# Performance work log

Hardware: AMD Instinct MI355X
Metric: run time of the kernel (lower is better)

## Reference

```python
import jax, jax.numpy as jnp
import numpy as np
import math

DIM = 512
HEADS = 8
DH = DIM // HEADS
B, C, H, W = 2, 512, 48, 48


def setup_inputs() -> dict:
    key = jax.random.key(0)
    k1, k2, k3, k4 = jax.random.split(key, 4)
    x = jax.random.normal(k1, (B, C, H, W), dtype=jnp.float32)
    # torch Linear weights: [out_features, in_features]
    w_qkv = jax.random.normal(k2, (3 * DIM, DIM), dtype=jnp.float32) * (DIM ** -0.5)
    w_out = jax.random.normal(k3, (DIM, DIM), dtype=jnp.float32) * (DIM ** -0.5)
    b_out = jax.random.normal(k4, (DIM,), dtype=jnp.float32) * 0.01
    wavelength = jnp.asarray(0.1, dtype=jnp.float32)
    return {"x": x, "w_qkv": w_qkv, "w_out": w_out, "b_out": b_out, "wavelength": wavelength}


def reference(x, w_qkv, w_out, b_out, wavelength):
    b, c, h, w = x.shape
    n = h * w
    scale = DH ** -0.5

    x_flat = x.reshape(b, c, n).transpose(0, 2, 1)  # [B, N, C]
    qkv = jnp.einsum('bnc,dc->bnd', x_flat, w_qkv)   # [B, N, 3*DIM]
    q, k, v = jnp.split(qkv, 3, axis=-1)

    def to_heads(t):
        return t.reshape(b, n, HEADS, DH).transpose(0, 2, 1, 3)  # [B, h, N, dh]

    q, k, v = to_heads(q), to_heads(k), to_heads(v)

    dots = jnp.einsum('bhid,bhjd->bhij', q, k) * scale  # [B, h, N, N]

    # Fresnel interference bias over spatial positions
    yy, xx = jnp.meshgrid(jnp.arange(h), jnp.arange(w), indexing='ij')
    positions = jnp.stack([yy, xx], axis=-1).astype(jnp.float32).reshape(-1, 2)  # [N, 2]
    pos_diff = positions[None, :, :] - positions[:, None, :]  # [N, N, 2]
    distances = jnp.sqrt(jnp.sum(pos_diff ** 2, axis=-1) + 1e-8)  # [N, N]
    phase = 2.0 * math.pi * distances / (jnp.abs(wavelength) * h + 1e-6)
    interference = jnp.cos(phase)

    dots = dots + interference[None, None, :, :] * 0.1
    attn = jax.nn.softmax(dots, axis=-1)
    out = jnp.einsum('bhij,bhjd->bhid', attn, v)  # [B, h, N, dh]
    out = out.transpose(0, 2, 1, 3).reshape(b, n, HEADS * DH)  # [B, N, DIM]
    out = jnp.einsum('bnd,od->bno', out, w_out) + b_out
    return out.transpose(0, 2, 1).reshape(b, c, h, w)
```

## Files before the change

### kernel.cpp

```cpp
#include <hip/hip_runtime.h>
#include <math.h>

#define BB 2
#define CC 512
#define NN 2304
#define NH 8
#define DD 512
#define D3 1536
#define WIDTH 48
#define C1 0.18033688f

#define KSPLIT 2
#define KTILES 18
#define NTBL 213

typedef _Float16 h8 __attribute__((ext_vector_type(8)));
typedef _Float16 h4 __attribute__((ext_vector_type(4)));
typedef _Float16 h2 __attribute__((ext_vector_type(2)));
typedef float f4 __attribute__((ext_vector_type(4)));

__device__ __forceinline__ void gload16(const void* g, void* s) {
  __builtin_amdgcn_global_load_lds(
      (const __attribute__((address_space(1))) unsigned int*)g,
      (__attribute__((address_space(3))) unsigned int*)s, 16, 0, 0);
}

__global__ __launch_bounds__(256) void prep_k(
    const float* __restrict__ x, const float* __restrict__ wq,
    const float* __restrict__ wo, const float* __restrict__ wavp,
    _Float16* __restrict__ xt, _Float16* __restrict__ wqh,
    _Float16* __restrict__ woh, _Float16* __restrict__ btf)
{
  __shared__ float Ls[32][33];
  const int t = threadIdx.x;
  const int e = blockIdx.x;

  if (e < 2304) {
    const int n0 = (e % 72) * 32;
    const int c0 = ((e / 72) % 16) * 32;
    const int b  = e / 1152;
#pragma unroll
    for (int p = 0; p < 4; ++p) {
      const int cl = (t >> 5) + p * 8, nl = t & 31;
      Ls[cl][nl] = x[((size_t)b * CC + c0 + cl) * NN + n0 + nl];
    }
    __syncthreads();
#pragma unroll
    for (int p = 0; p < 2; ++p) {
      const int nl = (t >> 4) + p * 16, cl = (t & 15) * 2;
      h2 v = {(_Float16)Ls[cl][nl], (_Float16)Ls[cl + 1][nl]};
      *(h2*)(xt + ((size_t)b * NN + n0 + nl) * CC + c0 + cl) = v;
    }
  } else if (e < 3328) {
    const int idx = (e - 2304) * 256 + t;
    const int NQ = (D3 * CC) / 4;
    if (idx < NQ) {
      float4 v = *(const float4*)(wq + (size_t)idx * 4);
      h4 o = {(_Float16)v.x, (_Float16)v.y, (_Float16)v.z, (_Float16)v.w};
      *(h4*)(wqh + (size_t)idx * 4) = o;
    } else {
      const int j = idx - NQ;
      float4 v = *(const float4*)(wo + (size_t)j * 4);
      h4 o = {(_Float16)v.x, (_Float16)v.y, (_Float16)v.z, (_Float16)v.w};
      *(h4*)(woh + (size_t)j * 4) = o;
    }
  } else {
    const int tbl = (e - 3328) * 2 + (t >> 7);
    if (tbl < NTBL) {
      const int tid = t & 127;
      const int dD = tbl / 3, qm = tbl % 3;
      const int qt0 = qm + 36;
      const int kt0 = qt0 - (dD - 35);
      const int w = tid >> 6, quad = (tid >> 4) & 3, l15 = tid & 15;
      const float pc = 6.283185307179586f / (fabsf(wavp[0]) * (float)WIDTH + 1e-6f);
      _Float16* o = btf + ((size_t)tbl * 128 + tid) * 32;
#pragma unroll
      for (int g = 0; g < 4; ++g) {
        h8 v;
#pragma unroll
        for (int el = 0; el < 8; ++el) {
          const int j = g * 8 + el;
          const int nt = j >> 4, mt = (j >> 2) & 3, r = j & 3;
          const int q = qt0 * 64 + w * 32 + nt * 16 + l15;
          const int k = kt0 * 64 + mt * 16 + quad * 4 + r;
          const float dy = (float)(q / WIDTH) - (float)(k / WIDTH);
          const float dx = (float)(q % WIDTH) - (float)(k % WIDTH);
          const float dist = sqrtf(dy * dy + dx * dx + 1e-8f);
          v[el] = (_Float16)(0.1f * __cosf(dist * pc) * 1.44269504f);
        }
        *(h8*)(o + g * 8) = v;
      }
    }
  }
}

__global__ __launch_bounds__(256) void qkv_gemm_k(
    const _Float16* __restrict__ xt, const _Float16* __restrict__ wqh,
    _Float16* __restrict__ qb, _Float16* __restrict__ kb,
    _Float16* __restrict__ vb)
{
  __shared__ _Float16 Xs[128][32];
  __shared__ _Float16 Ws[128][32];
  const int t = threadIdx.x;
  const int lane = t & 63, w = t >> 6;
  const int l15 = lane & 15, quad = lane >> 4;
  const int wm = w & 1, wn = w >> 1;
  const int n0 = blockIdx.x * 128;
  const int d0 = blockIdx.y * 128;
  const int b  = blockIdx.z;
  const bool isv = (d0 >= 2 * DD);
  const _Float16* xb = xt + (size_t)b * NN * CC;

  const int srow = lane >> 2, scol = (lane & 3) * 8;

  f4 acc[4][4];
#pragma unroll
  for (int mt = 0; mt < 4; ++mt)
#pragma unroll
    for (int nt = 0; nt < 4; ++nt) acc[mt][nt] = (f4)(0.f);

  for (int c0 = 0; c0 < CC; c0 += 32) {
#pragma unroll
    for (int r = 0; r < 2; ++r) {
      const int ci = w + r * 4;
      const int row = ci * 16 + srow;
      gload16(xb + (size_t)(n0 + row) * CC + c0 + scol, &Xs[0][0] + ci * 512);
      gload16(wqh + (size_t)(d0 + row) * CC + c0 + scol, &Ws[0][0] + ci * 512);
    }
    __syncthreads();

    h8 wfr[4], xfr[4];
#pragma unroll
    for (int mt = 0; mt < 4; ++mt)
      wfr[mt] = *(const h8*)&Ws[wm * 64 + mt * 16 + l15][quad * 8];
#pragma unroll
    for (int nt = 0; nt < 4; ++nt)
      xfr[nt] = *(const h8*)&Xs[wn * 64 + nt * 16 + l15][quad * 8];

    if (!isv) {
#pragma unroll
      for (int mt = 0; mt < 4; ++mt)
#pragma unroll
        for (int nt = 0; nt < 4; ++nt)
          acc[mt][nt] = __builtin_amdgcn_mfma_f32_16x16x32_f16(
              wfr[mt], xfr[nt], acc[mt][nt], 0, 0, 0);
    } else {
#pragma unroll
      for (int mt = 0; mt < 4; ++mt)
#pragma unroll
        for (int nt = 0; nt < 4; ++nt)
          acc[mt][nt] = __builtin_amdgcn_mfma_f32_16x16x32_f16(
              xfr[nt], wfr[mt], acc[mt][nt], 0, 0, 0);
    }
    __syncthreads();
  }

  if (!isv) {
    const int which = d0 >> 9;
    _Float16* buf = which == 0 ? qb : kb;
    const float qs = (which == 0) ? C1 : 1.0f;
    const int h = ((d0 & 511) >> 6) + wm;
#pragma unroll
    for (int mt = 0; mt < 4; ++mt) {
      const int dh = mt * 16 + quad * 4;
#pragma unroll
      for (int nt = 0; nt < 4; ++nt) {
        const int token = n0 + wn * 64 + nt * 16 + l15;
        h4 o = {(_Float16)(acc[mt][nt][0] * qs), (_Float16)(acc[mt][nt][1] * qs),
                (_Float16)(acc[mt][nt][2] * qs), (_Float16)(acc[mt][nt][3] * qs)};
        *(h4*)(buf + (((size_t)b * NH + h) * NN + token) * 64 + dh) = o;
      }
    }
  } else {
    const int h = ((d0 - 2 * DD) >> 6) + wm;
#pragma unroll
    for (int mt = 0; mt < 4; ++mt) {
      const int dh = mt * 16 + l15;
#pragma unroll
      for (int nt = 0; nt < 4; ++nt) {
        const int token = n0 + wn * 64 + nt * 16 + quad * 4;
        h4 o = {(_Float16)acc[mt][nt][0], (_Float16)acc[mt][nt][1],
                (_Float16)acc[mt][nt][2], (_Float16)acc[mt][nt][3]};
        *(h4*)(vb + (((size_t)b * NH + h) * 64 + dh) * NN + token) = o;
      }
    }
  }
}

__global__ __launch_bounds__(256, 4) void attn_k(
    const _Float16* __restrict__ qb, const _Float16* __restrict__ kb,
    const _Float16* __restrict__ vb, const _Float16* __restrict__ btf,
    _Float16* __restrict__ op, float* __restrict__ lp)
{
  __shared__ _Float16 Ks[64][72];
  __shared__ _Float16 Vs[64][72];
  __shared__ _Float16 Ps[128][72];

  const int t    = threadIdx.x;
  const int lane = t & 63;
  const int w    = t >> 6;
  const int l15  = lane & 15;
  const int quad = lane >> 4;
  const int qpair = blockIdx.x >> 1;
  const int kq    = blockIdx.x & 1;
  const int n0 = qpair * 128;
  const int qtile = qpair * 2 + (w >> 1);
  const int h  = blockIdx.y;
  const int b  = blockIdx.z;
  const size_t base = ((size_t)b * NH + h) * NN * 64;
  const _Float16* qp = qb + base;
  const _Float16* kp = kb + base;
  const _Float16* vp = vb + base;

  h8 qf[2][2];
#pragma unroll
  for (int nt = 0; nt < 2; ++nt)
#pragma unroll
    for (int ks = 0; ks < 2; ++ks)
      qf[nt][ks] = *(const h8*)(qp + (size_t)(n0 + w * 32 + nt * 16 + l15) * 64 +
                                ks * 32 + quad * 8);

  f4 oc[4][2];
#pragma unroll
  for (int mt = 0; mt < 4; ++mt)
#pragma unroll
    for (int nt = 0; nt < 2; ++nt) oc[mt][nt] = (f4)(0.f);
  float lac[2][2] = {};

  const _Float16* bp =
      btf + ((size_t)((qtile - kq * KTILES + 35) * 3 + qtile % 3) * 128 +
             (w & 1) * 64 + lane) * 32;

  for (int kt = 0; kt < KTILES; ++kt) {
    const int k0 = (kq * KTILES + kt) * 64;
    h8 kr[2], vr[2], bfr[4];
#pragma unroll
    for (int r = 0; r < 2; ++r) {
      const int c = t + r * 256;
      const int row = c >> 3, off = (c & 7) * 8;
      kr[r] = *(const h8*)(kp + (size_t)(k0 + row) * 64 + off);
      vr[r] = *(const h8*)(vp + (size_t)row * NN + k0 + off);
    }
#pragma unroll
    for (int r = 0; r < 4; ++r) bfr[r] = *(const h8*)(bp + r * 8);
    bp -= 3 * 128 * 32;
    __syncthreads();
#pragma unroll
    for (int r = 0; r < 2; ++r) {
      const int c = t + r * 256;
      const int row = c >> 3, off = (c & 7) * 8;
      *(h8*)&Ks[row][off] = kr[r];
      *(h8*)&Vs[row][off] = vr[r];
    }
    __syncthreads();

    f4 st[4][2];
#pragma unroll
    for (int mt = 0; mt < 4; ++mt)
#pragma unroll
      for (int nt = 0; nt < 2; ++nt) {
        const int jb = nt * 16 + mt * 4;
        f4 s = {(float)bfr[jb >> 3][(jb & 7) + 0],
                (float)bfr[jb >> 3][(jb & 7) + 1],
                (float)bfr[jb >> 3][(jb & 7) + 2],
                (float)bfr[jb >> 3][(jb & 7) + 3]};
        st[mt][nt] = s;
      }
#pragma unroll
    for (int ks = 0; ks < 2; ++ks) {
#pragma unroll
      for (int mt = 0; mt < 4; ++mt) {
        h8 kf = *(const h8*)&Ks[mt * 16 + l15][ks * 32 + quad * 8];
#pragma unroll
        for (int nt = 0; nt < 2; ++nt)
          st[mt][nt] = __builtin_amdgcn_mfma_f32_16x16x32_f16(
              kf, qf[nt][ks], st[mt][nt], 0, 0, 0);
      }
    }

#pragma unroll
    for (int nt = 0; nt < 2; ++nt) {
      const int q = w * 32 + nt * 16 + l15;
#pragma unroll
      for (int mt = 0; mt < 4; ++mt) {
        const float p0 = __builtin_exp2f(st[mt][nt][0]);
        const float p1 = __builtin_exp2f(st[mt][nt][1]);
        const float p2 = __builtin_exp2f(st[mt][nt][2]);
        const float p3 = __builtin_exp2f(st[mt][nt][3]);
        lac[nt][0] += p0 + p1;
        lac[nt][1] += p2 + p3;
        const auto plo = __builtin_amdgcn_cvt_pkrtz(p0, p1);
        const auto phi = __builtin_amdgcn_cvt_pkrtz(p2, p3);
        h4 pk = {(_Float16)plo[0], (_Float16)plo[1],
                 (_Float16)phi[0], (_Float16)phi[1]};
        *(h4*)&Ps[q][mt * 16 + quad * 4] = pk;
      }
    }

#pragma unroll
    for (int ks = 0; ks < 2; ++ks) {
      h8 pf[2];
#pragma unroll
      for (int nt = 0; nt < 2; ++nt)
        pf[nt] = *(const h8*)&Ps[w * 32 + nt * 16 + l15][ks * 32 + quad * 8];
#pragma unroll
      for (int mt = 0; mt < 4; ++mt) {
        h8 vf = *(const h8*)&Vs[mt * 16 + l15][ks * 32 + quad * 8];
#pragma unroll
        for (int nt = 0; nt < 2; ++nt)
          oc[mt][nt] = __builtin_amdgcn_mfma_f32_16x16x32_f16(
              vf, pf[nt], oc[mt][nt], 0, 0, 0);
      }
    }
  }

#pragma unroll
  for (int nt = 0; nt < 2; ++nt) {
    float l = lac[nt][0] + lac[nt][1];
    l += __shfl_xor(l, 16);
    l += __shfl_xor(l, 32);
    const float inv = 1.f / l;
    const int qi = n0 + w * 32 + nt * 16 + l15;
    _Float16* od = op + (size_t)kq * BB * NN * DD +
                   ((size_t)b * NN + qi) * DD + h * 64;
#pragma unroll
    for (int mt = 0; mt < 4; ++mt) {
      const int dh = mt * 16 + quad * 4;
      h4 o = {(_Float16)(oc[mt][nt][0] * inv), (_Float16)(oc[mt][nt][1] * inv),
              (_Float16)(oc[mt][nt][2] * inv), (_Float16)(oc[mt][nt][3] * inv)};
      *(h4*)(od + dh) = o;
    }
    if (quad == 0)
      lp[(size_t)kq * BB * NH * NN + ((size_t)b * NH + h) * NN + qi] = l;
  }
}

__global__ __launch_bounds__(256) void comb_k(
    const _Float16* __restrict__ op, const float* __restrict__ lp,
    _Float16* __restrict__ ho)
{
  const int idx = blockIdx.x * 256 + threadIdx.x;
  const int d8 = idx & 63;
  const int bn = idx >> 6;
  const int n = bn % NN, b = bn / NN;
  const int h = d8 >> 3;
  const size_t SL = (size_t)BB * NH * NN;
  const size_t SO = (size_t)BB * NN * DD;
  const size_t li = ((size_t)b * NH + h) * NN + n;
  const float l0 = lp[li];
  const float l1 = lp[SL + li];
  const float inv = 1.f / (l0 + l1);
  const float w0 = l0 * inv, w1 = l1 * inv;
  h8 o0 = *(const h8*)(op + (size_t)bn * DD + d8 * 8);
  h8 o1 = *(const h8*)(op + SO + (size_t)bn * DD + d8 * 8);
  h8 r;
#pragma unroll
  for (int i = 0; i < 8; ++i)
    r[i] = (_Float16)((float)o0[i] * w0 + (float)o1[i] * w1);
  *(h8*)(ho + (size_t)bn * DD + d8 * 8) = r;
}

__global__ __launch_bounds__(64) void out_gemm_k(
    const _Float16* __restrict__ ho, const _Float16* __restrict__ woh,
    const float* __restrict__ bias, float* __restrict__ out)
{
  __shared__ _Float16 Hs[64][32];
  __shared__ _Float16 Ws2[64][32];
  const int t = threadIdx.x;
  const int l15 = t & 15, quad = t >> 4;
  const int n0 = blockIdx.x * 64;
  const int o0 = blockIdx.y * 64;
  const int b  = blockIdx.z;
  const int srow = t >> 2, scol = (t & 3) * 8;

  f4 acc[4][4];
#pragma unroll
  for (int mt = 0; mt < 4; ++mt)
#pragma unroll
    for (int nt = 0; nt < 4; ++nt) acc[mt][nt] = (f4)(0.f);

  for (int c0 = 0; c0 < DD; c0 += 32) {
#pragma unroll
    for (int ci = 0; ci < 4; ++ci) {
      const int row = ci * 16 + srow;
      gload16(ho + ((size_t)b * NN + n0 + row) * DD + c0 + scol,
              &Hs[0][0] + ci * 512);
      gload16(woh + (size_t)(o0 + row) * DD + c0 + scol,
              &Ws2[0][0] + ci * 512);
    }
    __syncthreads();
    h8 hf[4], wf[4];
#pragma unroll
    for (int mt = 0; mt < 4; ++mt)
      hf[mt] = *(const h8*)&Hs[mt * 16 + l15][quad * 8];
#pragma unroll
    for (int nt = 0; nt < 4; ++nt)
      wf[nt] = *(const h8*)&Ws2[nt * 16 + l15][quad * 8];
#pragma unroll
    for (int mt = 0; mt < 4; ++mt)
#pragma unroll
      for (int nt = 0; nt < 4; ++nt)
        acc[mt][nt] = __builtin_amdgcn_mfma_f32_16x16x32_f16(
            hf[mt], wf[nt], acc[mt][nt], 0, 0, 0);
    __syncthreads();
  }

#pragma unroll
  for (int nt = 0; nt < 4; ++nt) {
    const int o = o0 + nt * 16 + l15;
    const float bv = bias[o];
#pragma unroll
    for (int mt = 0; mt < 4; ++mt) {
      const int token = n0 + mt * 16 + quad * 4;
      float4 v = {acc[mt][nt][0] + bv, acc[mt][nt][1] + bv,
                  acc[mt][nt][2] + bv, acc[mt][nt][3] + bv};
      *(float4*)(out + ((size_t)b * DD + o) * NN + token) = v;
    }
  }
}

extern "C" void kernel_launch(void* const* d_in, const int* in_sizes, int n_in,
                              void* d_out, int out_size, void* d_ws, size_t ws_size,
                              hipStream_t stream)
{
  (void)in_sizes; (void)n_in; (void)out_size; (void)ws_size;
  const float* x     = (const float*)d_in[0];
  const float* w_qkv = (const float*)d_in[1];
  const float* w_out = (const float*)d_in[2];
  const float* b_out = (const float*)d_in[3];
  const float* wav   = (const float*)d_in[4];
  float* out = (float*)d_out;

  const size_t SZ  = (size_t)BB * NH * NN * 64;
  const size_t BTF = (size_t)NTBL * 128 * 32;

  _Float16* qb  = (_Float16*)d_ws;
  _Float16* kb  = qb + SZ;
  _Float16* vb  = kb + SZ;
  _Float16* btf = vb + SZ;
  _Float16* op  = btf + BTF;
  float*    lpf = (float*)(op + 2 * SZ);
  _Float16* woh = (_Float16*)(lpf + 2 * (size_t)BB * NH * NN);
  _Float16* ho  = qb;
  _Float16* xt  = op;
  _Float16* wqh = op + SZ;

  prep_k    <<<dim3(2304 + 1024 + 107), 256, 0, stream>>>(x, w_qkv, w_out, wav,
                                                          xt, wqh, woh, btf);
  qkv_gemm_k<<<dim3(NN / 128, D3 / 128, BB), 256, 0, stream>>>(xt, wqh, qb, kb, vb);
  attn_k    <<<dim3((NN / 128) * KSPLIT, NH, BB), 256, 0, stream>>>(qb, kb, vb, btf, op, lpf);
  comb_k    <<<dim3((BB * NN * 64) / 256), 256, 0, stream>>>(op, lpf, ho);
  out_gemm_k<<<dim3(NN / 64, DD / 64, BB), 64, 0, stream>>>(ho, woh, b_out, out);
}
```

Before: 161.5 us.

## Use single-wave attention blocks loading K/V fragments directly from global

The attention kernel now launches one 64-thread wave per 32-query tile instead of four waves sharing K/V tiles through LDS. Each wave loads its K and V MFMA fragments straight from global memory, which removes the LDS staging and both __syncthreads per key tile. A swizzled linear block index groups blocks across XCDs so that those sharing a batch and head land together. The trade-off is that K/V reuse across query tiles now depends on L2/cache rather than shared memory, and global loads are issued four times as often.

New measurement: 193.7 us. 1.2x slower.

```diff
diff --git a/kernel.cpp b/kernel.cpp
--- a/kernel.cpp
+++ b/kernel.cpp
@@ -187,26 +187,27 @@
   }
 }
 
-__global__ __launch_bounds__(256, 4) void attn_k(
+__global__ __launch_bounds__(64, 2) void attn_k(
     const _Float16* __restrict__ qb, const _Float16* __restrict__ kb,
     const _Float16* __restrict__ vb, const _Float16* __restrict__ btf,
     _Float16* __restrict__ op, float* __restrict__ lp)
 {
-  __shared__ _Float16 Ks[64][72];
-  __shared__ _Float16 Vs[64][72];
-  __shared__ _Float16 Ps[128][72];
+  __shared__ _Float16 Ps[32][72];
 
   const int t    = threadIdx.x;
-  const int lane = t & 63;
-  const int w    = t >> 6;
-  const int l15  = lane & 15;
-  const int quad = lane >> 4;
-  const int qpair = blockIdx.x >> 1;
-  const int kq    = blockIdx.x & 1;
-  const int n0 = qpair * 128;
-  const int qtile = qpair * 2 + (w >> 1);
-  const int h  = blockIdx.y;
-  const int b  = blockIdx.z;
+  const int l15  = t & 15;
+  const int quad = t >> 4;
+
+  const int lin  = blockIdx.x;
+  const int id   = (lin & 7) * 288 + (lin >> 3);
+  const int bh   = id / 144;
+  const int rem  = id - bh * 144;
+  const int kq   = rem / 72;
+  const int qw   = rem - kq * 72;
+  const int b    = bh >> 3, h = bh & 7;
+  const int q0   = qw * 32;
+  const int qtile = qw >> 1;
+
   const size_t base = ((size_t)b * NH + h) * NN * 64;
   const _Float16* qp = qb + base;
   const _Float16* kp = kb + base;
@@ -217,7 +218,7 @@
   for (int nt = 0; nt < 2; ++nt)
 #pragma unroll
     for (int ks = 0; ks < 2; ++ks)
-      qf[nt][ks] = *(const h8*)(qp + (size_t)(n0 + w * 32 + nt * 16 + l15) * 64 +
+      qf[nt][ks] = *(const h8*)(qp + (size_t)(q0 + nt * 16 + l15) * 64 +
                                 ks * 32 + quad * 8);
 
   f4 oc[4][2];
@@ -227,32 +228,24 @@
     for (int nt = 0; nt < 2; ++nt) oc[mt][nt] = (f4)(0.f);
   float lac[2][2] = {};
 
+  const int ktg0 = kq * KTILES;
   const _Float16* bp =
-      btf + ((size_t)((qtile - kq * KTILES + 35) * 3 + qtile % 3) * 128 +
-             (w & 1) * 64 + lane) * 32;
+      btf + ((size_t)((qtile - ktg0 + 35) * 3 + qtile % 3) * 128 +
+             (qw & 1) * 64 + t) * 32;
 
   for (int kt = 0; kt < KTILES; ++kt) {
-    const int k0 = (kq * KTILES + kt) * 64;
-    h8 kr[2], vr[2], bfr[4];
-#pragma unroll
-    for (int r = 0; r < 2; ++r) {
-      const int c = t + r * 256;
-      const int row = c >> 3, off = (c & 7) * 8;
-      kr[r] = *(const h8*)(kp + (size_t)(k0 + row) * 64 + off);
-      vr[r] = *(const h8*)(vp + (size_t)row * NN + k0 + off);
-    }
+    const int k0 = (ktg0 + kt) * 64;
+
+    h8 kf[2][4], bfr[4];
+#pragma unroll
+    for (int ks = 0; ks < 2; ++ks)
+#pragma unroll
+      for (int mt = 0; mt < 4; ++mt)
+        kf[ks][mt] = *(const h8*)(kp + (size_t)(k0 + mt * 16 + l15) * 64 +
+                                  ks * 32 + quad * 8);
 #pragma unroll
     for (int r = 0; r < 4; ++r) bfr[r] = *(const h8*)(bp + r * 8);
     bp -= 3 * 128 * 32;
-    __syncthreads();
-#pragma unroll
-    for (int r = 0; r < 2; ++r) {
-      const int c = t + r * 256;
-      const int row = c >> 3, off = (c & 7) * 8;
-      *(h8*)&Ks[row][off] = kr[r];
-      *(h8*)&Vs[row][off] = vr[r];
-    }
-    __syncthreads();
 
     f4 st[4][2];
 #pragma unroll
@@ -266,21 +259,27 @@
                 (float)bfr[jb >> 3][(jb & 7) + 3]};
         st[mt][nt] = s;
       }
-#pragma unroll
-    for (int ks = 0; ks < 2; ++ks) {
-#pragma unroll
-      for (int mt = 0; mt < 4; ++mt) {
-        h8 kf = *(const h8*)&Ks[mt * 16 + l15][ks * 32 + quad * 8];
+
+#pragma unroll
+    for (int ks = 0; ks < 2; ++ks)
+#pragma unroll
+      for (int mt = 0; mt < 4; ++mt)
 #pragma unroll
         for (int nt = 0; nt < 2; ++nt)
           st[mt][nt] = __builtin_amdgcn_mfma_f32_16x16x32_f16(
-              kf, qf[nt][ks], st[mt][nt], 0, 0, 0);
-      }
-    }
+              kf[ks][mt], qf[nt][ks], st[mt][nt], 0, 0, 0);
+
+    h8 vf[2][4];
+#pragma unroll
+    for (int ks = 0; ks < 2; ++ks)
+#pragma unroll
+      for (int mt = 0; mt < 4; ++mt)
+        vf[ks][mt] = *(const h8*)(vp + (size_t)(mt * 16 + l15) * NN + k0 +
+                                  ks * 32 + quad * 8);
 
 #pragma unroll
     for (int nt = 0; nt < 2; ++nt) {
-      const int q = w * 32 + nt * 16 + l15;
+      const int q = nt * 16 + l15;
 #pragma unroll
       for (int mt = 0; mt < 4; ++mt) {
         const float p0 = __builtin_exp2f(st[mt][nt][0]);
@@ -302,15 +301,13 @@
       h8 pf[2];
 #pragma unroll
       for (int nt = 0; nt < 2; ++nt)
-        pf[nt] = *(const h8*)&Ps[w * 32 + nt * 16 + l15][ks * 32 + quad * 8];
-#pragma unroll
-      for (int mt = 0; mt < 4; ++mt) {
-        h8 vf = *(const h8*)&Vs[mt * 16 + l15][ks * 32 + quad * 8];
+        pf[nt] = *(const h8*)&Ps[nt * 16 + l15][ks * 32 + quad * 8];
+#pragma unroll
+      for (int mt = 0; mt < 4; ++mt)
 #pragma unroll
         for (int nt = 0; nt < 2; ++nt)
           oc[mt][nt] = __builtin_amdgcn_mfma_f32_16x16x32_f16(
-              vf, pf[nt], oc[mt][nt], 0, 0, 0);
-      }
+              vf[ks][mt], pf[nt], oc[mt][nt], 0, 0, 0);
     }
   }
 
@@ -320,7 +317,7 @@
     l += __shfl_xor(l, 16);
     l += __shfl_xor(l, 32);
     const float inv = 1.f / l;
-    const int qi = n0 + w * 32 + nt * 16 + l15;
+    const int qi = q0 + nt * 16 + l15;
     _Float16* od = op + (size_t)kq * BB * NN * DD +
                    ((size_t)b * NN + qi) * DD + h * 64;
 #pragma unroll
@@ -448,7 +445,7 @@
   prep_k    <<<dim3(2304 + 1024 + 107), 256, 0, stream>>>(x, w_qkv, w_out, wav,
                                                           xt, wqh, woh, btf);
   qkv_gemm_k<<<dim3(NN / 128, D3 / 128, BB), 256, 0, stream>>>(xt, wqh, qb, kb, vb);
-  attn_k    <<<dim3((NN / 128) * KSPLIT, NH, BB), 256, 0, stream>>>(qb, kb, vb, btf, op, lpf);
+  attn_k    <<<dim3(2304), 64, 0, stream>>>(qb, kb, vb, btf, op, lpf);
   comb_k    <<<dim3((BB * NN * 64) / 256), 256, 0, stream>>>(op, lpf, ho);
   out_gemm_k<<<dim3(NN / 64, DD / 64, BB), 64, 0, stream>>>(ho, woh, b_out, out);
 }
```
